# Kernel tuning notes

Hardware: AMD Instinct MI355X
Metric: run time of the kernel (lower is better)

The kernel has to match this reference:

```python
import jax, jax.numpy as jnp
import numpy as np

D_MODEL = 1024
NUM_HEADS = 16
D_K = D_MODEL // NUM_HEADS


def setup_inputs() -> dict:
    key = jax.random.key(0)
    ks = jax.random.split(key, 5)
    s = 1.0 / np.sqrt(D_MODEL)
    return {
        "x": jax.random.normal(ks[0], (2, 2048, D_MODEL), dtype=jnp.float32),
        "Wq": jax.random.normal(ks[1], (D_MODEL, D_MODEL), dtype=jnp.float32) * s,
        "bq": jnp.zeros((D_MODEL,), jnp.float32),
        "Wk": jax.random.normal(ks[2], (D_MODEL, D_MODEL), dtype=jnp.float32) * s,
        "bk": jnp.zeros((D_MODEL,), jnp.float32),
        "Wv": jax.random.normal(ks[3], (D_MODEL, D_MODEL), dtype=jnp.float32) * s,
        "bv": jnp.zeros((D_MODEL,), jnp.float32),
        "Wo": jax.random.normal(ks[4], (D_MODEL, D_MODEL), dtype=jnp.float32) * s,
        "bo": jnp.zeros((D_MODEL,), jnp.float32),
    }


def _rotate_half(t):
    t1, t2 = t[..., : D_K // 2], t[..., D_K // 2 :]
    return jnp.concatenate((-t2, t1), axis=-1)


def reference(x, Wq, bq, Wk, bk, Wv, bv, Wo, bo):
    B, S, D = x.shape
    H, dk = NUM_HEADS, D_K
    # RoPE tables: inv_freq over even dims, emb = cat(freqs, freqs)
    inv_freq = 1.0 / (10000.0 ** (jnp.arange(0, dk, 2, dtype=jnp.float32) / dk))
    pos = jnp.arange(S, dtype=jnp.float32)
    freqs = pos[:, None] * inv_freq[None, :]            # [S, dk/2]
    emb = jnp.concatenate((freqs, freqs), axis=-1)      # [S, dk]
    cos = jnp.cos(emb)[None, :, None, :]                # [1, S, 1, dk]
    sin = jnp.sin(emb)[None, :, None, :]

    q = (x @ Wq + bq).reshape(B, S, H, dk)
    k = (x @ Wk + bk).reshape(B, S, H, dk)
    v = (x @ Wv + bv).reshape(B, S, H, dk)

    q = q * cos + _rotate_half(q) * sin
    k = k * cos + _rotate_half(k) * sin

    # [B,H,S,S] scores, stable softmax, then weighted sum of V
    scores = jnp.einsum("bqhd,bkhd->bhqk", q, k) / jnp.sqrt(jnp.float32(dk))
    attn = jax.nn.softmax(scores, axis=-1)
    out = jnp.einsum("bhqk,bkhd->bqhd", attn, v).reshape(B, S, D)
    return out @ Wo + bo
```

## Files before the change

### kernel.cpp

```cpp
#include <hip/hip_runtime.h>
#include <hip/hip_bf16.h>
#include <math.h>

typedef __bf16 bf16_t;
typedef bf16_t bf16x4 __attribute__((ext_vector_type(4)));
typedef bf16_t bf16x8 __attribute__((ext_vector_type(8)));
typedef float f32x4 __attribute__((ext_vector_type(4)));

#define SEQ 2048
#define BATCH 2
#define NHEAD 16
#define DK 64
#define DMODEL 1024

#define GLOAD16(gsrc, ldst)                                                        \
    __builtin_amdgcn_global_load_lds(                                              \
        (const __attribute__((address_space(1))) void*)(gsrc),                     \
        (__attribute__((address_space(3))) void*)(ldst), 16, 0, 0)

__device__ __forceinline__ float exp2_hw(float x) {
#if __has_builtin(__builtin_amdgcn_exp2f)
    return __builtin_amdgcn_exp2f(x);
#else
    float r; asm("v_exp_f32 %0, %1" : "=v"(r) : "v"(x)); return r;
#endif
}

__global__ __launch_bounds__(256)
void prep_kernel(const float* __restrict__ x, bf16_t* __restrict__ y,
                 const float* __restrict__ W0, const float* __restrict__ W1,
                 const float* __restrict__ W2, const float* __restrict__ W3,
                 bf16_t* __restrict__ Wt, float2* __restrict__ cs) {
    __shared__ float t[32][33];
    const int id = blockIdx.x, tid = threadIdx.x;
    if (id < 4096) {
        int i = (id * 256 + tid) * 4;
        float4 v = *reinterpret_cast<const float4*>(x + i);
        bf16x4 o = { (bf16_t)v.x, (bf16_t)v.y, (bf16_t)v.z, (bf16_t)v.w };
        *reinterpret_cast<bf16x4*>(y + i) = o;
    } else if (id < 8192) {
        const int id2 = id - 4096;
        const int z = id2 >> 10, rem = id2 & 1023;
        const int n0 = (rem & 31) * 32, k0 = ((rem >> 5) & 31) * 32;
        const int tx = tid & 31, ty = tid >> 5;
        const float* W = (z == 0) ? W0 : (z == 1) ? W1 : (z == 2) ? W2 : W3;
        bf16_t* out = Wt + ((size_t)z << 20);
#pragma unroll
        for (int i = 0; i < 32; i += 8)
            t[ty + i][tx] = W[(size_t)(k0 + ty + i) * DMODEL + n0 + tx];
        __syncthreads();
#pragma unroll
        for (int i = 0; i < 32; i += 8)
            out[(size_t)(n0 + ty + i) * DMODEL + k0 + tx] = (bf16_t)t[tx][ty + i];
    } else {
        int idx = (id - 8192) * 256 + tid;
        int j = idx & 31, s = idx >> 5;
        float inv = powf(10000.0f, -(float)j / 32.0f);
        float ang = (float)s * inv;
        cs[idx] = make_float2(cosf(ang), sinf(ang));
    }
}

template<int NF>
__device__ __forceinline__ void gemm_core(const bf16_t* __restrict__ A,
                                          const bf16_t* __restrict__ Bt,
                                          int m0, int n0,
                                          bf16_t* As, bf16_t* Bs,
                                          f32x4 (&acc)[4][NF]) {
    const int tid = threadIdx.x, lane = tid & 63, wid = tid >> 6;
    const int wr = wid >> 1, wc = wid & 1;
    const int lm = lane & 15, lq = lane >> 4;
    constexpr int BROWS = NF * 32;
    constexpr int NT = DMODEL / 32;

    const int r_in = lane >> 2;
    const int csw  = (((lane & 3) ^ ((lane >> 3) & 3)) << 3);
    const bf16_t* Ag = A  + (size_t)(m0 + 32 * wid + r_in) * DMODEL + csw;
    const bf16_t* Bg = Bt + (size_t)(n0 + (NF * 8) * wid + r_in) * DMODEL + csw;
    const int cswr = ((lq ^ ((lm >> 1) & 3)) << 4);

    auto stage = [&](int t, int buf) {
        const int k0 = t * 32;
        bf16_t* a = As + buf * (128 * 32) + 32 * wid * 32;
        bf16_t* b = Bs + buf * (BROWS * 32) + (NF * 8) * wid * 32;
        GLOAD16(Ag + k0,               a);
        GLOAD16(Ag + 16 * DMODEL + k0, a + 16 * 32);
        GLOAD16(Bg + k0,               b);
        if constexpr (NF == 4) GLOAD16(Bg + 16 * DMODEL + k0, b + 16 * 32);
    };

    stage(0, 0);
    stage(1, 1);
    int cb = 0;
    for (int t = 0; t < NT; ++t) {
        if (t + 2 < NT) {
            int sb = cb + 2; if (sb >= 3) sb -= 3;
            stage(t + 2, sb);
            if constexpr (NF == 4) asm volatile("s_waitcnt vmcnt(8)" ::: "memory");
            else                   asm volatile("s_waitcnt vmcnt(6)" ::: "memory");
        } else if (t + 1 < NT) {
            if constexpr (NF == 4) asm volatile("s_waitcnt vmcnt(4)" ::: "memory");
            else                   asm volatile("s_waitcnt vmcnt(3)" ::: "memory");
        } else {
            asm volatile("s_waitcnt vmcnt(0)" ::: "memory");
        }
        __builtin_amdgcn_s_barrier();

        const char* pAs = (const char*)(As + cb * (128 * 32));
        const char* pBs = (const char*)(Bs + cb * (BROWS * 32));
        bf16x8 af[4], bfr[NF];
#pragma unroll
        for (int mf = 0; mf < 4; ++mf)
            af[mf] = *reinterpret_cast<const bf16x8*>(pAs + (wr * 64 + mf * 16 + lm) * 64 + cswr);
#pragma unroll
        for (int nf = 0; nf < NF; ++nf)
            bfr[nf] = *reinterpret_cast<const bf16x8*>(pBs + (wc * (NF * 16) + nf * 16 + lm) * 64 + cswr);
#pragma unroll
        for (int mf = 0; mf < 4; ++mf)
#pragma unroll
            for (int nf = 0; nf < NF; ++nf)
                acc[mf][nf] = __builtin_amdgcn_mfma_f32_16x16x32_bf16(af[mf], bfr[nf], acc[mf][nf], 0, 0, 0);

        asm volatile("" ::: "memory");
        __builtin_amdgcn_s_barrier();
        if (++cb == 3) cb = 0;
    }
}

__global__ __launch_bounds__(256)
void gemm_qkv_kernel(const bf16_t* __restrict__ xb, const bf16_t* __restrict__ wtqk,
                     const bf16_t* __restrict__ wtv,
                     const float* __restrict__ bq, const float* __restrict__ bk,
                     const float* __restrict__ bv,
                     bf16_t* __restrict__ qb, bf16_t* __restrict__ kb,
                     bf16_t* __restrict__ vtb, const float2* __restrict__ cs) {
    __shared__ bf16_t As[3 * 128 * 32];
    __shared__ bf16_t Bs[3 * 128 * 32];
    const int tid = threadIdx.x, lane = tid & 63, wid = tid >> 6;
    const int wr = wid >> 1, wc = wid & 1;
    const int lm = lane & 15, lq = lane >> 4;
    const int orig = blockIdx.x;
    const int id = (orig & 7) * 96 + (orig >> 3);
    f32x4 acc[4][4] = {};

    if (id < 512) {
        const int m0 = (id >> 4) * 128, n0 = (id & 15) * 128;
        gemm_core<4>(xb, wtqk, m0, n0, As, Bs, acc);
        const bool is_k = (n0 >= 1024);
        const float* bs = is_k ? bk : bq;
        bf16_t* C = is_k ? kb : qb;
        const int cb = (is_k ? n0 - 1024 : n0) + wc * 64;
        const float b0 = bs[cb + lm],      b1 = bs[cb + 16 + lm];
        const float b2 = bs[cb + 32 + lm], b3 = bs[cb + 48 + lm];
#pragma unroll
        for (int mf = 0; mf < 4; ++mf)
#pragma unroll
            for (int i = 0; i < 4; ++i) {
                const int row = m0 + wr * 64 + mf * 16 + lq * 4 + i;
                const int s = row & (SEQ - 1);
                const float2 cs0 = cs[s * 32 + lm];
                const float2 cs1 = cs[s * 32 + 16 + lm];
                const float a0 = acc[mf][0][i] + b0, a1 = acc[mf][1][i] + b1;
                const float a2 = acc[mf][2][i] + b2, a3 = acc[mf][3][i] + b3;
                bf16_t* p = C + (size_t)row * DMODEL + cb;
                p[lm]      = (bf16_t)(a0 * cs0.x - a2 * cs0.y);
                p[16 + lm] = (bf16_t)(a1 * cs1.x - a3 * cs1.y);
                p[32 + lm] = (bf16_t)(a2 * cs0.x + a0 * cs0.y);
                p[48 + lm] = (bf16_t)(a3 * cs1.x + a1 * cs1.y);
            }
    } else {
        const int id2 = id - 512;
        const int m0 = (id2 & 7) * 128, n0 = (id2 >> 3) * 128;
        gemm_core<4>(wtv, xb, m0, n0, As, Bs, acc);
#pragma unroll
        for (int mf = 0; mf < 4; ++mf)
#pragma unroll
            for (int i = 0; i < 4; ++i) {
                const int row = m0 + wr * 64 + mf * 16 + lq * 4 + i;
                const float brow = bv[row];
#pragma unroll
                for (int nf = 0; nf < 4; ++nf) {
                    const int col = n0 + wc * 64 + nf * 16 + lm;
                    vtb[(size_t)row * 4096 + col] = (bf16_t)(acc[mf][nf][i] + brow);
                }
            }
    }
}

__global__ __launch_bounds__(256)
void gemm_out_kernel(const bf16_t* __restrict__ A, const bf16_t* __restrict__ Bt,
                     const float* __restrict__ bias, float* __restrict__ C) {
    __shared__ bf16_t As[3 * 128 * 32];
    __shared__ bf16_t Bs[3 * 64 * 32];
    const int tid = threadIdx.x, lane = tid & 63, wid = tid >> 6;
    const int wr = wid >> 1, wc = wid & 1;
    const int lm = lane & 15, lq = lane >> 4;
    const int orig = blockIdx.x;
    const int id = (orig & 7) * 64 + (orig >> 3);
    const int m0 = (id >> 4) * 128, n0 = (id & 15) * 64;
    f32x4 acc[4][2] = {};
    gemm_core<2>(A, Bt, m0, n0, As, Bs, acc);
#pragma unroll
    for (int nf = 0; nf < 2; ++nf) {
        const int col = n0 + wc * 32 + nf * 16 + lm;
        const float bcol = bias[col];
#pragma unroll
        for (int mf = 0; mf < 4; ++mf)
#pragma unroll
            for (int i = 0; i < 4; ++i) {
                const int row = m0 + wr * 64 + mf * 16 + lq * 4 + i;
                C[(size_t)row * DMODEL + col] = acc[mf][nf][i] + bcol;
            }
    }
}

__global__ __launch_bounds__(256)
void attn_kernel(const bf16_t* __restrict__ q, const bf16_t* __restrict__ k,
                 const bf16_t* __restrict__ vt, bf16_t* __restrict__ attnout) {
    const int tid = threadIdx.x, lane = tid & 63, wid = tid >> 6;
    const int lm = lane & 15, lq = lane >> 4;
    const int bh = blockIdx.y, b = bh >> 4, h = bh & 15;
    const int qrow0 = blockIdx.x * 128 + wid * 32;
    const float MS = 20.0f;

    __shared__ bf16_t Ks[2][64][64];
    __shared__ bf16_t Vs[2][64][64];

    const bf16_t* qA = q + ((size_t)(b * SEQ + qrow0 + lm) * NHEAD + h) * DK + lq * 8;
    const bf16_t* qB = qA + (size_t)16 * NHEAD * DK;
    bf16x8 aqA0 = *reinterpret_cast<const bf16x8*>(qA);
    bf16x8 aqA1 = *reinterpret_cast<const bf16x8*>(qA + 32);
    bf16x8 aqB0 = *reinterpret_cast<const bf16x8*>(qB);
    bf16x8 aqB1 = *reinterpret_cast<const bf16x8*>(qB + 32);
#pragma unroll
    for (int j = 0; j < 8; ++j) {
        aqA0[j] = (bf16_t)((float)aqA0[j] * 0.18033688f);
        aqA1[j] = (bf16_t)((float)aqA1[j] * 0.18033688f);
        aqB0[j] = (bf16_t)((float)aqB0[j] * 0.18033688f);
        aqB1[j] = (bf16_t)((float)aqB1[j] * 0.18033688f);
    }
    const bf16_t one = (bf16_t)1.0f;
    const bf16x8 ones = { one, one, one, one, one, one, one, one };
    const f32x4 cinit = { -MS, -MS, -MS, -MS };

    const int r0   = 8 * wid + (lane >> 3);
    const int scol = (((lane & 7) ^ (lane >> 3)) << 3);
    const int sig  = ((r0 >> 2) & 3) * 8 + ((r0 >> 4) & 1) * 4 + (r0 & 3);
    const bf16_t* kg = k  + ((size_t)(b * SEQ + sig) * NHEAD + h) * DK + scol;
    const bf16_t* vg = vt + ((size_t)(h * DK + r0)) * 4096 + (size_t)b * SEQ + scol;
    const size_t kstep = (size_t)NHEAD * DK;
    const char* ksb = (const char*)Ks;
    const char* vsb = (const char*)Vs;
    const int c0 = (lq << 4) ^ ((lm & 7) << 4);
    const int rowb = lm * 128;

    f32x4 OA[4] = {}, OB[4] = {};
    f32x4 olA = {}, olB = {};

    auto stage = [&](int buf, int kb) {
        GLOAD16(kg + (size_t)kb * kstep,        &Ks[buf][8 * wid][0]);
        GLOAD16(kg + (size_t)(kb + 32) * kstep, &Ks[buf][32 + 8 * wid][0]);
        GLOAD16(vg + kb,                        &Vs[buf][8 * wid][0]);
        GLOAD16(vg + (size_t)32 * 4096 + kb,    &Vs[buf][32 + 8 * wid][0]);
    };

    stage(0, 0);

    int buf = 0;
    for (int kb = 0; kb < SEQ; kb += 64) {
        if (kb + 64 < SEQ) {
            stage(buf ^ 1, kb + 64);
            asm volatile("s_waitcnt vmcnt(4)" ::: "memory");
        } else {
            asm volatile("s_waitcnt vmcnt(0)" ::: "memory");
        }
        __builtin_amdgcn_s_barrier();
        asm volatile("" ::: "memory");

        const char* kt  = ksb + buf * 8192;
        const char* vtl = vsb + buf * 8192;

        f32x4 stA[4], stB[4];
        __builtin_amdgcn_s_setprio(1);
#pragma unroll
        for (int t = 0; t < 4; ++t) {
            bf16x8 a0 = *reinterpret_cast<const bf16x8*>(kt + t * 2048 + rowb + c0);
            bf16x8 a1 = *reinterpret_cast<const bf16x8*>(kt + t * 2048 + rowb + (c0 ^ 64));
            f32x4 sA = __builtin_amdgcn_mfma_f32_16x16x32_bf16(a0, aqA0, cinit, 0, 0, 0);
            sA = __builtin_amdgcn_mfma_f32_16x16x32_bf16(a1, aqA1, sA, 0, 0, 0);
            f32x4 sB = __builtin_amdgcn_mfma_f32_16x16x32_bf16(a0, aqB0, cinit, 0, 0, 0);
            sB = __builtin_amdgcn_mfma_f32_16x16x32_bf16(a1, aqB1, sB, 0, 0, 0);
            stA[t] = sA; stB[t] = sB;
        }
        __builtin_amdgcn_s_setprio(0);

        bf16x8 paA0, paA1, paB0, paB1;
#pragma unroll
        for (int t = 0; t < 2; ++t)
#pragma unroll
            for (int i = 0; i < 4; ++i) {
                paA0[4 * t + i] = (bf16_t)exp2_hw(stA[t][i]);
                paA1[4 * t + i] = (bf16_t)exp2_hw(stA[t + 2][i]);
                paB0[4 * t + i] = (bf16_t)exp2_hw(stB[t][i]);
                paB1[4 * t + i] = (bf16_t)exp2_hw(stB[t + 2][i]);
            }

        __builtin_amdgcn_s_setprio(1);
#pragma unroll
        for (int nf = 0; nf < 4; ++nf) {
            bf16x8 v0 = *reinterpret_cast<const bf16x8*>(vtl + nf * 2048 + rowb + c0);
            bf16x8 v1 = *reinterpret_cast<const bf16x8*>(vtl + nf * 2048 + rowb + (c0 ^ 64));
            f32x4 oA = OA[nf], oB = OB[nf];
            oA = __builtin_amdgcn_mfma_f32_16x16x32_bf16(v0, paA0, oA, 0, 0, 0);
            oA = __builtin_amdgcn_mfma_f32_16x16x32_bf16(v1, paA1, oA, 0, 0, 0);
            oB = __builtin_amdgcn_mfma_f32_16x16x32_bf16(v0, paB0, oB, 0, 0, 0);
            oB = __builtin_amdgcn_mfma_f32_16x16x32_bf16(v1, paB1, oB, 0, 0, 0);
            OA[nf] = oA; OB[nf] = oB;
        }
        olA = __builtin_amdgcn_mfma_f32_16x16x32_bf16(ones, paA0, olA, 0, 0, 0);
        olA = __builtin_amdgcn_mfma_f32_16x16x32_bf16(ones, paA1, olA, 0, 0, 0);
        olB = __builtin_amdgcn_mfma_f32_16x16x32_bf16(ones, paB0, olB, 0, 0, 0);
        olB = __builtin_amdgcn_mfma_f32_16x16x32_bf16(ones, paB1, olB, 0, 0, 0);
        __builtin_amdgcn_s_setprio(0);

        asm volatile("" ::: "memory");
        __builtin_amdgcn_s_barrier();
        buf ^= 1;
    }

    const float invA = 1.0f / olA[0];
    const float invB = 1.0f / olB[0];
    bf16_t* obA = attnout + ((size_t)(b * SEQ + qrow0 + lm) * NHEAD + h) * DK;
    bf16_t* obB = obA + (size_t)16 * NHEAD * DK;
#pragma unroll
    for (int nf = 0; nf < 4; ++nf) {
        bf16x4 cA = { (bf16_t)(OA[nf][0] * invA), (bf16_t)(OA[nf][1] * invA),
                      (bf16_t)(OA[nf][2] * invA), (bf16_t)(OA[nf][3] * invA) };
        bf16x4 cB = { (bf16_t)(OB[nf][0] * invB), (bf16_t)(OB[nf][1] * invB),
                      (bf16_t)(OB[nf][2] * invB), (bf16_t)(OB[nf][3] * invB) };
        *reinterpret_cast<bf16x4*>(obA + nf * 16 + lq * 4) = cA;
        *reinterpret_cast<bf16x4*>(obB + nf * 16 + lq * 4) = cB;
    }
}

extern "C" void kernel_launch(void* const* d_in, const int* in_sizes, int n_in,
                              void* d_out, int out_size, void* d_ws, size_t ws_size,
                              hipStream_t stream) {
    const float* x  = (const float*)d_in[0];
    const float* Wq = (const float*)d_in[1];
    const float* bq = (const float*)d_in[2];
    const float* Wk = (const float*)d_in[3];
    const float* bk = (const float*)d_in[4];
    const float* Wv = (const float*)d_in[5];
    const float* bv = (const float*)d_in[6];
    const float* Wo = (const float*)d_in[7];
    const float* bo = (const float*)d_in[8];
    float* out = (float*)d_out;

    char* ws = (char*)d_ws;
    bf16_t* xb  = (bf16_t*)(ws);
    bf16_t* wtq = (bf16_t*)(ws + ((size_t)8  << 20));
    bf16_t* wtv = wtq + (2 << 20);
    bf16_t* wto = wtq + (3 << 20);
    bf16_t* qb  = (bf16_t*)(ws + ((size_t)16 << 20));
    bf16_t* kb  = (bf16_t*)(ws + ((size_t)24 << 20));
    bf16_t* vtb = (bf16_t*)(ws + ((size_t)32 << 20));
    float2* csT = (float2*)(ws + ((size_t)40 << 20));
    bf16_t* aob = xb;

    prep_kernel<<<8448, 256, 0, stream>>>(x, xb, Wq, Wk, Wv, Wo, wtq, csT);
    gemm_qkv_kernel<<<768, 256, 0, stream>>>(xb, wtq, wtv, bq, bk, bv, qb, kb, vtb, csT);
    attn_kernel<<<dim3(16, 32), 256, 0, stream>>>(qb, kb, vtb, aob);
    gemm_out_kernel<<<512, 256, 0, stream>>>(aob, wto, bo, out);
}
```

Measured before the change: 124.8 us.

## Load K/V fragments directly from global into registers, dropping LDS staging

The attention kernel stops staging K and V tiles through double-buffered shared memory with async global-to-LDS loads and barriers. Each wave now loads its own K and V MFMA fragments straight from global memory into registers, prefetching the next K tile while the softmax exp runs. This removes the block barriers and LDS traffic. In exchange, each of the four waves re-reads the same K/V data from global memory and L2 (no sharing across waves), and the loads are less coalesced.

```diff
diff --git a/kernel.cpp b/kernel.cpp
--- a/kernel.cpp
+++ b/kernel.cpp
@@ -223,9 +223,6 @@
     const int qrow0 = blockIdx.x * 128 + wid * 32;
     const float MS = 20.0f;
 
-    __shared__ bf16_t Ks[2][64][64];
-    __shared__ bf16_t Vs[2][64][64];
-
     const bf16_t* qA = q + ((size_t)(b * SEQ + qrow0 + lm) * NHEAD + h) * DK + lq * 8;
     const bf16_t* qB = qA + (size_t)16 * NHEAD * DK;
     bf16x8 aqA0 = *reinterpret_cast<const bf16x8*>(qA);
@@ -243,56 +240,55 @@
     const bf16x8 ones = { one, one, one, one, one, one, one, one };
     const f32x4 cinit = { -MS, -MS, -MS, -MS };
 
-    const int r0   = 8 * wid + (lane >> 3);
-    const int scol = (((lane & 7) ^ (lane >> 3)) << 3);
-    const int sig  = ((r0 >> 2) & 3) * 8 + ((r0 >> 4) & 1) * 4 + (r0 & 3);
-    const bf16_t* kg = k  + ((size_t)(b * SEQ + sig) * NHEAD + h) * DK + scol;
-    const bf16_t* vg = vt + ((size_t)(h * DK + r0)) * 4096 + (size_t)b * SEQ + scol;
-    const size_t kstep = (size_t)NHEAD * DK;
-    const char* ksb = (const char*)Ks;
-    const char* vsb = (const char*)Vs;
-    const int c0 = (lq << 4) ^ ((lm & 7) << 4);
-    const int rowb = lm * 128;
+    const int rbase = 8 * (lm >> 2) + (lm & 3);
+    const int tofs[4] = { 0, 4, 32, 36 };
+    const bf16_t* kp[4];
+#pragma unroll
+    for (int t = 0; t < 4; ++t)
+        kp[t] = k + ((size_t)(b * SEQ + tofs[t] + rbase) * NHEAD + h) * DK + lq * 8;
+    const bf16_t* vp[4];
+#pragma unroll
+    for (int nf = 0; nf < 4; ++nf)
+        vp[nf] = vt + (size_t)(h * DK + nf * 16 + lm) * 4096 + b * SEQ + lq * 8;
 
     f32x4 OA[4] = {}, OB[4] = {};
     f32x4 olA = {}, olB = {};
 
-    auto stage = [&](int buf, int kb) {
-        GLOAD16(kg + (size_t)kb * kstep,        &Ks[buf][8 * wid][0]);
-        GLOAD16(kg + (size_t)(kb + 32) * kstep, &Ks[buf][32 + 8 * wid][0]);
-        GLOAD16(vg + kb,                        &Vs[buf][8 * wid][0]);
-        GLOAD16(vg + (size_t)32 * 4096 + kb,    &Vs[buf][32 + 8 * wid][0]);
-    };
-
-    stage(0, 0);
-
-    int buf = 0;
+    bf16x8 kf0[4], kf1[4];
+#pragma unroll
+    for (int t = 0; t < 4; ++t) {
+        kf0[t] = *reinterpret_cast<const bf16x8*>(kp[t]);
+        kf1[t] = *reinterpret_cast<const bf16x8*>(kp[t] + 32);
+    }
+
     for (int kb = 0; kb < SEQ; kb += 64) {
-        if (kb + 64 < SEQ) {
-            stage(buf ^ 1, kb + 64);
-            asm volatile("s_waitcnt vmcnt(4)" ::: "memory");
-        } else {
-            asm volatile("s_waitcnt vmcnt(0)" ::: "memory");
-        }
-        __builtin_amdgcn_s_barrier();
-        asm volatile("" ::: "memory");
-
-        const char* kt  = ksb + buf * 8192;
-        const char* vtl = vsb + buf * 8192;
+        bf16x8 vf0[4], vf1[4];
+#pragma unroll
+        for (int nf = 0; nf < 4; ++nf) {
+            vf0[nf] = *reinterpret_cast<const bf16x8*>(vp[nf] + kb);
+            vf1[nf] = *reinterpret_cast<const bf16x8*>(vp[nf] + kb + 32);
+        }
 
         f32x4 stA[4], stB[4];
         __builtin_amdgcn_s_setprio(1);
 #pragma unroll
         for (int t = 0; t < 4; ++t) {
-            bf16x8 a0 = *reinterpret_cast<const bf16x8*>(kt + t * 2048 + rowb + c0);
-            bf16x8 a1 = *reinterpret_cast<const bf16x8*>(kt + t * 2048 + rowb + (c0 ^ 64));
-            f32x4 sA = __builtin_amdgcn_mfma_f32_16x16x32_bf16(a0, aqA0, cinit, 0, 0, 0);
-            sA = __builtin_amdgcn_mfma_f32_16x16x32_bf16(a1, aqA1, sA, 0, 0, 0);
-            f32x4 sB = __builtin_amdgcn_mfma_f32_16x16x32_bf16(a0, aqB0, cinit, 0, 0, 0);
-            sB = __builtin_amdgcn_mfma_f32_16x16x32_bf16(a1, aqB1, sB, 0, 0, 0);
+            f32x4 sA = __builtin_amdgcn_mfma_f32_16x16x32_bf16(kf0[t], aqA0, cinit, 0, 0, 0);
+            sA = __builtin_amdgcn_mfma_f32_16x16x32_bf16(kf1[t], aqA1, sA, 0, 0, 0);
+            f32x4 sB = __builtin_amdgcn_mfma_f32_16x16x32_bf16(kf0[t], aqB0, cinit, 0, 0, 0);
+            sB = __builtin_amdgcn_mfma_f32_16x16x32_bf16(kf1[t], aqB1, sB, 0, 0, 0);
             stA[t] = sA; stB[t] = sB;
         }
         __builtin_amdgcn_s_setprio(0);
+
+        if (kb + 64 < SEQ) {
+            const size_t adv = (size_t)(kb + 64) * NHEAD * DK;
+#pragma unroll
+            for (int t = 0; t < 4; ++t) {
+                kf0[t] = *reinterpret_cast<const bf16x8*>(kp[t] + adv);
+                kf1[t] = *reinterpret_cast<const bf16x8*>(kp[t] + adv + 32);
+            }
+        }
 
         bf16x8 paA0, paA1, paB0, paB1;
 #pragma unroll
@@ -308,13 +304,11 @@
         __builtin_amdgcn_s_setprio(1);
 #pragma unroll
         for (int nf = 0; nf < 4; ++nf) {
-            bf16x8 v0 = *reinterpret_cast<const bf16x8*>(vtl + nf * 2048 + rowb + c0);
-            bf16x8 v1 = *reinterpret_cast<const bf16x8*>(vtl + nf * 2048 + rowb + (c0 ^ 64));
             f32x4 oA = OA[nf], oB = OB[nf];
-            oA = __builtin_amdgcn_mfma_f32_16x16x32_bf16(v0, paA0, oA, 0, 0, 0);
-            oA = __builtin_amdgcn_mfma_f32_16x16x32_bf16(v1, paA1, oA, 0, 0, 0);
-            oB = __builtin_amdgcn_mfma_f32_16x16x32_bf16(v0, paB0, oB, 0, 0, 0);
-            oB = __builtin_amdgcn_mfma_f32_16x16x32_bf16(v1, paB1, oB, 0, 0, 0);
+            oA = __builtin_amdgcn_mfma_f32_16x16x32_bf16(vf0[nf], paA0, oA, 0, 0, 0);
+            oA = __builtin_amdgcn_mfma_f32_16x16x32_bf16(vf1[nf], paA1, oA, 0, 0, 0);
+            oB = __builtin_amdgcn_mfma_f32_16x16x32_bf16(vf0[nf], paB0, oB, 0, 0, 0);
+            oB = __builtin_amdgcn_mfma_f32_16x16x32_bf16(vf1[nf], paB1, oB, 0, 0, 0);
             OA[nf] = oA; OB[nf] = oB;
         }
         olA = __builtin_amdgcn_mfma_f32_16x16x32_bf16(ones, paA0, olA, 0, 0, 0);
@@ -322,10 +316,6 @@
         olB = __builtin_amdgcn_mfma_f32_16x16x32_bf16(ones, paB0, olB, 0, 0, 0);
         olB = __builtin_amdgcn_mfma_f32_16x16x32_bf16(ones, paB1, olB, 0, 0, 0);
         __builtin_amdgcn_s_setprio(0);
-
-        asm volatile("" ::: "memory");
-        __builtin_amdgcn_s_barrier();
-        buf ^= 1;
     }
 
     const float invA = 1.0f / olA[0];
```

Result: slower. 195.7 us (+56.8%).

## Software-pipeline attention loop: compute next QK before current softmax/PV with 4-deep LDS ring

Applied to the files above, without the earlier changes.

Restructures the attention inner loop so the QK^T MFMAs for tile t+1 are issued before the exp2 and PV MFMAs of tile t, letting exp work overlap with matrix work. The LDS buffers grow from a 2-deep to a 4-deep ring, prefetching two tiles ahead, and the trailing barrier per iteration is removed. This doubles shared memory per block and adds register pressure from holding two sets of score fragments, which could reduce occupancy or cause spills.

```diff
diff --git a/kernel.cpp b/kernel.cpp
--- a/kernel.cpp
+++ b/kernel.cpp
@@ -222,9 +222,10 @@
     const int bh = blockIdx.y, b = bh >> 4, h = bh & 15;
     const int qrow0 = blockIdx.x * 128 + wid * 32;
     const float MS = 20.0f;
-
-    __shared__ bf16_t Ks[2][64][64];
-    __shared__ bf16_t Vs[2][64][64];
+    constexpr int NT = SEQ / 64;
+
+    __shared__ bf16_t Ks[4][64][64];
+    __shared__ bf16_t Vs[4][64][64];
 
     const bf16_t* qA = q + ((size_t)(b * SEQ + qrow0 + lm) * NHEAD + h) * DK + lq * 8;
     const bf16_t* qB = qA + (size_t)16 * NHEAD * DK;
@@ -263,48 +264,55 @@
         GLOAD16(vg + kb,                        &Vs[buf][8 * wid][0]);
         GLOAD16(vg + (size_t)32 * 4096 + kb,    &Vs[buf][32 + 8 * wid][0]);
     };
-
-    stage(0, 0);
-
-    int buf = 0;
-    for (int kb = 0; kb < SEQ; kb += 64) {
-        if (kb + 64 < SEQ) {
-            stage(buf ^ 1, kb + 64);
-            asm volatile("s_waitcnt vmcnt(4)" ::: "memory");
-        } else {
-            asm volatile("s_waitcnt vmcnt(0)" ::: "memory");
-        }
-        __builtin_amdgcn_s_barrier();
-        asm volatile("" ::: "memory");
-
-        const char* kt  = ksb + buf * 8192;
-        const char* vtl = vsb + buf * 8192;
-
-        f32x4 stA[4], stB[4];
+    auto qk = [&](int buf, f32x4 (&sA)[4], f32x4 (&sB)[4]) {
+        const char* kt = ksb + buf * 8192;
         __builtin_amdgcn_s_setprio(1);
 #pragma unroll
         for (int t = 0; t < 4; ++t) {
             bf16x8 a0 = *reinterpret_cast<const bf16x8*>(kt + t * 2048 + rowb + c0);
             bf16x8 a1 = *reinterpret_cast<const bf16x8*>(kt + t * 2048 + rowb + (c0 ^ 64));
-            f32x4 sA = __builtin_amdgcn_mfma_f32_16x16x32_bf16(a0, aqA0, cinit, 0, 0, 0);
-            sA = __builtin_amdgcn_mfma_f32_16x16x32_bf16(a1, aqA1, sA, 0, 0, 0);
-            f32x4 sB = __builtin_amdgcn_mfma_f32_16x16x32_bf16(a0, aqB0, cinit, 0, 0, 0);
-            sB = __builtin_amdgcn_mfma_f32_16x16x32_bf16(a1, aqB1, sB, 0, 0, 0);
-            stA[t] = sA; stB[t] = sB;
+            f32x4 xA = __builtin_amdgcn_mfma_f32_16x16x32_bf16(a0, aqA0, cinit, 0, 0, 0);
+            xA = __builtin_amdgcn_mfma_f32_16x16x32_bf16(a1, aqA1, xA, 0, 0, 0);
+            f32x4 xB = __builtin_amdgcn_mfma_f32_16x16x32_bf16(a0, aqB0, cinit, 0, 0, 0);
+            xB = __builtin_amdgcn_mfma_f32_16x16x32_bf16(a1, aqB1, xB, 0, 0, 0);
+            sA[t] = xA; sB[t] = xB;
         }
         __builtin_amdgcn_s_setprio(0);
+    };
+
+    stage(0, 0);
+    stage(1, 64);
+    asm volatile("s_waitcnt vmcnt(4)" ::: "memory");
+    __builtin_amdgcn_s_barrier();
+    asm volatile("" ::: "memory");
+    f32x4 stA[4], stB[4];
+    qk(0, stA, stB);
+
+    for (int t = 0; t < NT; ++t) {
+        const int kb = t * 64;
+        if (t + 2 < NT) stage((t + 2) & 3, kb + 128);
+        if (t + 1 < NT) {
+            if (t + 2 < NT) asm volatile("s_waitcnt vmcnt(4)" ::: "memory");
+            else            asm volatile("s_waitcnt vmcnt(0)" ::: "memory");
+            __builtin_amdgcn_s_barrier();
+            asm volatile("" ::: "memory");
+        }
+
+        f32x4 nA[4], nB[4];
+        if (t + 1 < NT) qk((t + 1) & 3, nA, nB);
 
         bf16x8 paA0, paA1, paB0, paB1;
 #pragma unroll
-        for (int t = 0; t < 2; ++t)
+        for (int u = 0; u < 2; ++u)
 #pragma unroll
             for (int i = 0; i < 4; ++i) {
-                paA0[4 * t + i] = (bf16_t)exp2_hw(stA[t][i]);
-                paA1[4 * t + i] = (bf16_t)exp2_hw(stA[t + 2][i]);
-                paB0[4 * t + i] = (bf16_t)exp2_hw(stB[t][i]);
-                paB1[4 * t + i] = (bf16_t)exp2_hw(stB[t + 2][i]);
+                paA0[4 * u + i] = (bf16_t)exp2_hw(stA[u][i]);
+                paA1[4 * u + i] = (bf16_t)exp2_hw(stA[u + 2][i]);
+                paB0[4 * u + i] = (bf16_t)exp2_hw(stB[u][i]);
+                paB1[4 * u + i] = (bf16_t)exp2_hw(stB[u + 2][i]);
             }
 
+        const char* vtl = vsb + (t & 3) * 8192;
         __builtin_amdgcn_s_setprio(1);
 #pragma unroll
         for (int nf = 0; nf < 4; ++nf) {
@@ -323,9 +331,10 @@
         olB = __builtin_amdgcn_mfma_f32_16x16x32_bf16(ones, paB1, olB, 0, 0, 0);
         __builtin_amdgcn_s_setprio(0);
 
-        asm volatile("" ::: "memory");
-        __builtin_amdgcn_s_barrier();
-        buf ^= 1;
+        if (t + 1 < NT) {
+#pragma unroll
+            for (int i = 0; i < 4; ++i) { stA[i] = nA[i]; stB[i] = nB[i]; }
+        }
     }
 
     const float invA = 1.0f / olA[0];
```

Measured after the change: 123.0 us (median of 2 runs). Within noise of the previous version (-1.4%).
